# Performance work log

Measured on AMD Instinct MI355X. Metric: run time of the kernel, lower is better.

Reference implementation:

```python
import jax, jax.numpy as jnp
import numpy as np

B, D, U = 8192, 512, 512


def setup_inputs() -> dict:
    key = jax.random.key(0)
    ks = jax.random.split(key, 5)
    return {
        "inputs": jax.random.normal(ks[0], (B, D), dtype=jnp.float32),
        "h_tm1": jax.random.normal(ks[1], (B, U), dtype=jnp.float32),
        "c_tm1": jax.random.normal(ks[2], (B, U), dtype=jnp.float32),
        "kernel": jax.random.normal(ks[3], (D, 4 * U), dtype=jnp.float32) * (1.0 / np.sqrt(D)),
        "recurrent_kernel": jax.random.normal(ks[4], (U, 4 * U), dtype=jnp.float32) * (1.0 / np.sqrt(U)),
        "bias": jnp.zeros((4 * U,), dtype=jnp.float32),
    }


def reference(inputs, h_tm1, c_tm1, kernel, recurrent_kernel, bias):
    # z: [B, 4U] = x @ W + h @ R + b
    z = inputs @ kernel + h_tm1 @ recurrent_kernel + bias
    z0, z1, z2, z3 = jnp.split(z, 4, axis=1)
    i = jax.nn.sigmoid(z0)
    f = jax.nn.sigmoid(z1)
    g = jnp.tanh(z2)
    o = jax.nn.sigmoid(z3)
    c = f * c_tm1 + i * g
    h = o * jnp.tanh(c)
    return (h, h, c)
```

## Files before the change

### kernel.cpp

```cpp
#include <hip/hip_runtime.h>
#include <hip/hip_bf16.h>
#include <cstdint>
#include <cstddef>

#define BB 8192
#define UU 512
#define KPACK 1024
#define NPACK 2048

using frag16 = __attribute__((ext_vector_type(8))) short;
using f32x4  = __attribute__((ext_vector_type(4))) float;

__device__ inline float fast_sigmoid(float x) { return 1.0f / (1.0f + __expf(-x)); }
__device__ inline float fast_tanh(float x) {
  x = fminf(fmaxf(x, -15.f), 15.f);
  float e = __expf(-2.0f * x);
  return (1.0f - e) / (1.0f + e);
}

__device__ inline unsigned cvt2(float lo, float hi) {
  __hip_bfloat162 b = __float22bfloat162_rn(float2{lo, hi});
  union { __hip_bfloat162 b; unsigned u; } v; v.b = b;
  return v.u;
}

__global__ __launch_bounds__(256) void pack_kernel(const float* __restrict__ x,
                                                   const float* __restrict__ h,
                                                   const float* __restrict__ W,
                                                   const float* __restrict__ R,
                                                   short* __restrict__ Xp,
                                                   short* __restrict__ Bt) {
  if (blockIdx.x < 4096) {
    int idx = blockIdx.x * 256 + threadIdx.x;
    int row = idx >> 7;
    int k8  = (idx & 127) << 3;
    const float* src = (k8 < 512) ? (x + (size_t)row * 512 + k8)
                                  : (h + (size_t)row * 512 + (k8 - 512));
    float4 a = *(const float4*)(src);
    float4 b = *(const float4*)(src + 4);
    uint4 o;
    o.x = cvt2(a.x, a.y);
    o.y = cvt2(a.z, a.w);
    o.z = cvt2(b.x, b.y);
    o.w = cvt2(b.z, b.w);
    *(uint4*)(Xp + ((size_t)idx << 3)) = o;
  } else {
    __shared__ float tile[64][65];
    int b2 = blockIdx.x - 4096;
    int nb = (b2 & 31) * 64;
    int kb = (b2 >> 5) * 64;
    int t  = threadIdx.x;
#pragma unroll
    for (int rep = 0; rep < 16; ++rep) {
      int kr = rep * 4 + (t >> 6);
      int c  = t & 63;
      int kg = kb + kr;
      const float* s = (kg < 512) ? (W + (size_t)kg * 2048) : (R + (size_t)(kg - 512) * 2048);
      tile[c][kr] = s[nb + c];
    }
    __syncthreads();
#pragma unroll
    for (int rep = 0; rep < 4; ++rep) {
      int nn = rep * 16 + (t >> 4);
      int k4 = (t & 15) << 2;
      uint2 o;
      o.x = cvt2(tile[nn][k4 + 0], tile[nn][k4 + 1]);
      o.y = cvt2(tile[nn][k4 + 2], tile[nn][k4 + 3]);
      *(uint2*)(Bt + (size_t)(nb + nn) * 1024 + kb + k4) = o;
    }
  }
}

__global__ __launch_bounds__(256, 4) void lstm_mfma_kernel(
    const short* __restrict__ A,
    const short* __restrict__ Bt,
    const float* __restrict__ bias,
    const float* __restrict__ cprev,
    float* __restrict__ out)
{
  __shared__ short lds_a[128 * 64];
  __shared__ short lds_b[128 * 64];

  const int tid  = threadIdx.x;
  const int lane = tid & 63;
  const int wave = tid >> 6;
  const int wm = wave & 1, wn = wave >> 1;
  const int bm = blockIdx.x;
  const int bn = blockIdx.y;

  const int r8  = lane >> 3;
  const int kg  = lane & 7;
  const int kgx = kg ^ r8;

  const short* ga[4];
  const short* gb[4];
  int ls_off[4];
#pragma unroll
  for (int t = 0; t < 4; ++t) {
    int rowl = wave * 32 + t * 8 + r8;
    ga[t] = A + (size_t)(bm * 128 + rowl) * 1024 + kgx * 8;
    int u    = bn * 32 + ((rowl >> 6) << 4) + (rowl & 15);
    int gate = (rowl >> 4) & 3;
    gb[t] = Bt + (size_t)(gate * 512 + u) * 1024 + kgx * 8;
    ls_off[t] = (wave * 32 + t * 8) * 64;
  }

  const int q   = lane >> 4;
  const int c16 = lane & 15;
  const int mx  = c16 & 7;

  f32x4 acc[4][4];
#pragma unroll
  for (int i = 0; i < 4; ++i)
#pragma unroll
    for (int j = 0; j < 4; ++j)
      acc[i][j] = f32x4{0.f, 0.f, 0.f, 0.f};

  for (int kt = 0; kt < 16; ++kt) {
    const int k0 = kt * 64;
#pragma unroll
    for (int t = 0; t < 4; ++t)
      __builtin_amdgcn_global_load_lds(
          (const __attribute__((address_space(1))) void*)(ga[t] + k0),
          (__attribute__((address_space(3))) void*)(lds_a + ls_off[t]), 16, 0, 0);
#pragma unroll
    for (int t = 0; t < 4; ++t)
      __builtin_amdgcn_global_load_lds(
          (const __attribute__((address_space(1))) void*)(gb[t] + k0),
          (__attribute__((address_space(3))) void*)(lds_b + ls_off[t]), 16, 0, 0);
    __syncthreads();
#pragma unroll
    for (int s = 0; s < 2; ++s) {
      const int kch = (((s << 2) + q) ^ mx) << 3;
      frag16 af[4], bf[4];
#pragma unroll
      for (int i = 0; i < 4; ++i)
        af[i] = *(const frag16*)(lds_a + (wm * 64 + i * 16 + c16) * 64 + kch);
#pragma unroll
      for (int j = 0; j < 4; ++j)
        bf[j] = *(const frag16*)(lds_b + (wn * 64 + j * 16 + c16) * 64 + kch);
#pragma unroll
      for (int i = 0; i < 4; ++i)
#pragma unroll
        for (int j = 0; j < 4; ++j)
          acc[i][j] = __builtin_amdgcn_mfma_f32_16x16x32_bf16(af[i], bf[j], acc[i][j], 0, 0, 0);
    }
    __syncthreads();
  }

  const int u = bn * 32 + wn * 16 + c16;
  const float b0 = bias[u];
  const float b1 = bias[512 + u];
  const float b2 = bias[1024 + u];
  const float b3 = bias[1536 + u];
  float* outh0 = out;
  float* outh1 = out + (size_t)BB * UU;
  float* outc  = out + (size_t)2 * BB * UU;

#pragma unroll
  for (int i = 0; i < 4; ++i) {
    int row0 = bm * 128 + wm * 64 + i * 16 + q * 4;
#pragma unroll
    for (int r = 0; r < 4; ++r) {
      size_t off = (size_t)(row0 + r) * UU + u;
      float z0 = acc[i][0][r] + b0;
      float z1 = acc[i][1][r] + b1;
      float z2 = acc[i][2][r] + b2;
      float z3 = acc[i][3][r] + b3;
      float ig = fast_sigmoid(z0);
      float fg = fast_sigmoid(z1);
      float gg = fast_tanh(z2);
      float og = fast_sigmoid(z3);
      float cp = cprev[off];
      float cc = fg * cp + ig * gg;
      float hh = og * fast_tanh(cc);
      outh0[off] = hh;
      outh1[off] = hh;
      outc[off]  = cc;
    }
  }
}

extern "C" void kernel_launch(void* const* d_in, const int* in_sizes, int n_in,
                              void* d_out, int out_size, void* d_ws, size_t ws_size,
                              hipStream_t stream) {
  const float* x  = (const float*)d_in[0];
  const float* h  = (const float*)d_in[1];
  const float* c  = (const float*)d_in[2];
  const float* W  = (const float*)d_in[3];
  const float* R  = (const float*)d_in[4];
  const float* b  = (const float*)d_in[5];
  float* out = (float*)d_out;

  short* Xp = (short*)d_ws;
  short* Bt = Xp + (size_t)BB * KPACK;

  pack_kernel<<<4608, 256, 0, stream>>>(x, h, W, R, Xp, Bt);
  lstm_mfma_kernel<<<dim3(64, 16), 256, 0, stream>>>(Xp, Bt, b, c, out);
}
```

Before: 148.0 us.

## Triple-buffer LDS with async prefetch and enlarge block tile to 256x128

The GEMM kernel now uses 512-thread blocks covering 256 rows by 128 columns, so each B tile is shared by twice as many A rows. K-tiles are staged through a three-deep LDS ring with global_load_lds prefetch two tiles ahead, governed by vmcnt waits and a single barrier per iteration instead of two syncthreads. MFMA sections are raised in priority with s_setprio. The aim is to hide global load latency and cut B-tile reloads, at the cost of about 144KB of LDS per block, which limits residency, and half as many blocks in the grid.

Result: slower. 154.5 us (+4.4%).

```diff
diff --git a/kernel.cpp b/kernel.cpp
--- a/kernel.cpp
+++ b/kernel.cpp
@@ -71,81 +71,105 @@
   }
 }
 
-__global__ __launch_bounds__(256, 4) void lstm_mfma_kernel(
+__global__ __launch_bounds__(512, 2) void lstm_mfma_kernel(
     const short* __restrict__ A,
     const short* __restrict__ Bt,
     const float* __restrict__ bias,
     const float* __restrict__ cprev,
     float* __restrict__ out)
 {
-  __shared__ short lds_a[128 * 64];
-  __shared__ short lds_b[128 * 64];
+  __shared__ short lds[3 * 24576];
 
   const int tid  = threadIdx.x;
   const int lane = tid & 63;
   const int wave = tid >> 6;
-  const int wm = wave & 1, wn = wave >> 1;
-  const int bm = blockIdx.x;
-  const int bn = blockIdx.y;
+  const int wm   = wave & 3;
+  const int wn   = wave >> 2;
+  const int bm   = blockIdx.x;
+  const int bn   = blockIdx.y;
 
   const int r8  = lane >> 3;
   const int kg  = lane & 7;
   const int kgx = kg ^ r8;
 
   const short* ga[4];
-  const short* gb[4];
-  int ls_off[4];
+  int la_off[4];
 #pragma unroll
   for (int t = 0; t < 4; ++t) {
     int rowl = wave * 32 + t * 8 + r8;
-    ga[t] = A + (size_t)(bm * 128 + rowl) * 1024 + kgx * 8;
+    ga[t] = A + (size_t)(bm * 256 + rowl) * 1024 + kgx * 8;
+    la_off[t] = (wave * 32 + t * 8) * 64;
+  }
+  const short* gb[2];
+  int lb_off[2];
+#pragma unroll
+  for (int t = 0; t < 2; ++t) {
+    int rowl = wave * 16 + t * 8 + r8;
     int u    = bn * 32 + ((rowl >> 6) << 4) + (rowl & 15);
     int gate = (rowl >> 4) & 3;
     gb[t] = Bt + (size_t)(gate * 512 + u) * 1024 + kgx * 8;
-    ls_off[t] = (wave * 32 + t * 8) * 64;
+    lb_off[t] = (wave * 16 + t * 8) * 64;
   }
 
   const int q   = lane >> 4;
   const int c16 = lane & 15;
   const int mx  = c16 & 7;
 
-  f32x4 acc[4][4];
-#pragma unroll
-  for (int i = 0; i < 4; ++i)
-#pragma unroll
-    for (int j = 0; j < 4; ++j)
-      acc[i][j] = f32x4{0.f, 0.f, 0.f, 0.f};
-
-  for (int kt = 0; kt < 16; ++kt) {
-    const int k0 = kt * 64;
+  auto STAGE = [&](int T, int bi) {
+    const int k0 = T * 64;
+    short* base = &lds[bi * 24576];
 #pragma unroll
     for (int t = 0; t < 4; ++t)
       __builtin_amdgcn_global_load_lds(
           (const __attribute__((address_space(1))) void*)(ga[t] + k0),
-          (__attribute__((address_space(3))) void*)(lds_a + ls_off[t]), 16, 0, 0);
-#pragma unroll
-    for (int t = 0; t < 4; ++t)
+          (__attribute__((address_space(3))) void*)(base + la_off[t]), 16, 0, 0);
+#pragma unroll
+    for (int t = 0; t < 2; ++t)
       __builtin_amdgcn_global_load_lds(
           (const __attribute__((address_space(1))) void*)(gb[t] + k0),
-          (__attribute__((address_space(3))) void*)(lds_b + ls_off[t]), 16, 0, 0);
-    __syncthreads();
-#pragma unroll
-    for (int s = 0; s < 2; ++s) {
-      const int kch = (((s << 2) + q) ^ mx) << 3;
-      frag16 af[4], bf[4];
+          (__attribute__((address_space(3))) void*)(base + 16384 + lb_off[t]), 16, 0, 0);
+  };
+
+  f32x4 acc[4][4];
+#pragma unroll
+  for (int i = 0; i < 4; ++i)
+#pragma unroll
+    for (int j = 0; j < 4; ++j)
+      acc[i][j] = f32x4{0.f, 0.f, 0.f, 0.f};
+
+  STAGE(0, 0);
+  STAGE(1, 1);
+
+  int rb = 0;
+  for (int T = 0; T < 16; ++T) {
+    if (T < 15) asm volatile("s_waitcnt vmcnt(6)" ::: "memory");
+    else        asm volatile("s_waitcnt vmcnt(0)" ::: "memory");
+    __builtin_amdgcn_s_barrier();
+    if (T + 2 < 16) {
+      int wb = rb + 2; if (wb >= 3) wb -= 3;
+      STAGE(T + 2, wb);
+    }
+    const short* la = &lds[rb * 24576];
+    const short* lb = la + 16384;
+    __builtin_amdgcn_s_setprio(1);
+#pragma unroll
+    for (int ks = 0; ks < 2; ++ks) {
+      const int ch8 = ((((ks << 2) + q) ^ mx) << 3);
+      frag16 af[4], bfv[4];
 #pragma unroll
       for (int i = 0; i < 4; ++i)
-        af[i] = *(const frag16*)(lds_a + (wm * 64 + i * 16 + c16) * 64 + kch);
+        af[i] = *(const frag16*)(la + (wm * 64 + i * 16 + c16) * 64 + ch8);
 #pragma unroll
       for (int j = 0; j < 4; ++j)
-        bf[j] = *(const frag16*)(lds_b + (wn * 64 + j * 16 + c16) * 64 + kch);
+        bfv[j] = *(const frag16*)(lb + (wn * 64 + j * 16 + c16) * 64 + ch8);
 #pragma unroll
       for (int i = 0; i < 4; ++i)
 #pragma unroll
         for (int j = 0; j < 4; ++j)
-          acc[i][j] = __builtin_amdgcn_mfma_f32_16x16x32_bf16(af[i], bf[j], acc[i][j], 0, 0, 0);
-    }
-    __syncthreads();
+          acc[i][j] = __builtin_amdgcn_mfma_f32_16x16x32_bf16(af[i], bfv[j], acc[i][j], 0, 0, 0);
+    }
+    __builtin_amdgcn_s_setprio(0);
+    rb = (rb == 2) ? 0 : rb + 1;
   }
 
   const int u = bn * 32 + wn * 16 + c16;
@@ -159,7 +183,7 @@
 
 #pragma unroll
   for (int i = 0; i < 4; ++i) {
-    int row0 = bm * 128 + wm * 64 + i * 16 + q * 4;
+    int row0 = bm * 256 + wm * 64 + i * 16 + q * 4;
 #pragma unroll
     for (int r = 0; r < 4; ++r) {
       size_t off = (size_t)(row0 + r) * UU + u;
@@ -196,5 +220,5 @@
   short* Bt = Xp + (size_t)BB * KPACK;
 
   pack_kernel<<<4608, 256, 0, stream>>>(x, h, W, R, Xp, Bt);
-  lstm_mfma_kernel<<<dim3(64, 16), 256, 0, stream>>>(Xp, Bt, b, c, out);
-}
+  lstm_mfma_kernel<<<dim3(32, 16), 512, 0, stream>>>(Xp, Bt, b, c, out);
+}
```

## Double-buffer LDS with K-tile 32 to overlap global loads with MFMA

Applied to the files above, without the earlier changes.

The GEMM main loop now uses two LDS buffers with K-tile 32 instead of one buffer with K-tile 64. The next tile's direct-to-LDS loads are issued before the current tile's MFMAs, waiting only with a partial vmcnt so loads overlap compute. A new XOR-swizzled layout packs two rows per 64-element line to keep LDS reads conflict-free. The cost is twice as many loop iterations and barriers. Synchronisation now depends on hand-placed s_barrier and vmcnt waits, which leaves correctness hinging on the exact count of outstanding loads.

After: 154.4 us. +4.3%, slower.

```diff
diff --git a/kernel.cpp b/kernel.cpp
--- a/kernel.cpp
+++ b/kernel.cpp
@@ -78,8 +78,7 @@
     const float* __restrict__ cprev,
     float* __restrict__ out)
 {
-  __shared__ short lds_a[128 * 64];
-  __shared__ short lds_b[128 * 64];
+  __shared__ short lds[2 * 8192];
 
   const int tid  = threadIdx.x;
   const int lane = tid & 63;
@@ -88,26 +87,47 @@
   const int bm = blockIdx.x;
   const int bn = blockIdx.y;
 
-  const int r8  = lane >> 3;
-  const int kg  = lane & 7;
-  const int kgx = kg ^ r8;
-
-  const short* ga[4];
-  const short* gb[4];
-  int ls_off[4];
-#pragma unroll
-  for (int t = 0; t < 4; ++t) {
-    int rowl = wave * 32 + t * 8 + r8;
-    ga[t] = A + (size_t)(bm * 128 + rowl) * 1024 + kgx * 8;
-    int u    = bn * 32 + ((rowl >> 6) << 4) + (rowl & 15);
-    int gate = (rowl >> 4) & 3;
-    gb[t] = Bt + (size_t)(gate * 512 + u) * 1024 + kgx * 8;
-    ls_off[t] = (wave * 32 + t * 8) * 64;
-  }
+  const int l8   = lane >> 3;
+  const int sl   = lane & 7;
+  const int slin = sl ^ l8;
+  const int rpar = slin >> 2;
+  const int cch  = slin & 3;
+
+  const short* ga0[2];
+  const short* gb0[2];
+  int la_off[2], lb_off[2];
+#pragma unroll
+  for (int i = 0; i < 2; ++i) {
+    int g    = wave * 2 + i;
+    int rloc = g * 16 + 2 * l8 + rpar;
+    ga0[i]    = A + (size_t)(bm * 128 + rloc) * 1024 + cch * 8;
+    la_off[i] = g * 512;
+    int u    = bn * 32 + ((rloc >> 6) << 4) + (rloc & 15);
+    int gate = (rloc >> 4) & 3;
+    gb0[i]    = Bt + (size_t)(gate * 512 + u) * 1024 + cch * 8;
+    lb_off[i] = 4096 + g * 512;
+  }
+
+  auto STAGE = [&](int kt, int bi) {
+    const int k0 = kt * 32;
+    short* base = &lds[bi * 8192];
+#pragma unroll
+    for (int i = 0; i < 2; ++i)
+      __builtin_amdgcn_global_load_lds(
+          (const __attribute__((address_space(1))) void*)(ga0[i] + k0),
+          (__attribute__((address_space(3))) void*)(base + la_off[i]), 16, 0, 0);
+#pragma unroll
+    for (int i = 0; i < 2; ++i)
+      __builtin_amdgcn_global_load_lds(
+          (const __attribute__((address_space(1))) void*)(gb0[i] + k0),
+          (__attribute__((address_space(3))) void*)(base + lb_off[i]), 16, 0, 0);
+  };
 
   const int q   = lane >> 4;
   const int c16 = lane & 15;
-  const int mx  = c16 & 7;
+  const int s_rd  = (((c16 & 1) << 2) | q) ^ (c16 >> 1);
+  const int aoff  = wm * 2048 + (c16 >> 1) * 64 + s_rd * 8;
+  const int boff  = 4096 + wn * 2048 + (c16 >> 1) * 64 + s_rd * 8;
 
   f32x4 acc[4][4];
 #pragma unroll
@@ -116,37 +136,33 @@
     for (int j = 0; j < 4; ++j)
       acc[i][j] = f32x4{0.f, 0.f, 0.f, 0.f};
 
-  for (int kt = 0; kt < 16; ++kt) {
-    const int k0 = kt * 64;
-#pragma unroll
-    for (int t = 0; t < 4; ++t)
-      __builtin_amdgcn_global_load_lds(
-          (const __attribute__((address_space(1))) void*)(ga[t] + k0),
-          (__attribute__((address_space(3))) void*)(lds_a + ls_off[t]), 16, 0, 0);
-#pragma unroll
-    for (int t = 0; t < 4; ++t)
-      __builtin_amdgcn_global_load_lds(
-          (const __attribute__((address_space(1))) void*)(gb[t] + k0),
-          (__attribute__((address_space(3))) void*)(lds_b + ls_off[t]), 16, 0, 0);
-    __syncthreads();
-#pragma unroll
-    for (int s = 0; s < 2; ++s) {
-      const int kch = (((s << 2) + q) ^ mx) << 3;
-      frag16 af[4], bf[4];
-#pragma unroll
-      for (int i = 0; i < 4; ++i)
-        af[i] = *(const frag16*)(lds_a + (wm * 64 + i * 16 + c16) * 64 + kch);
+  auto COMPUTE = [&](int kt) {
+    const short* base = &lds[(kt & 1) * 8192];
+    frag16 af[4], bfv[4];
+#pragma unroll
+    for (int i = 0; i < 4; ++i)
+      af[i] = *(const frag16*)(base + aoff + i * 512);
+#pragma unroll
+    for (int j = 0; j < 4; ++j)
+      bfv[j] = *(const frag16*)(base + boff + j * 512);
+#pragma unroll
+    for (int i = 0; i < 4; ++i)
 #pragma unroll
       for (int j = 0; j < 4; ++j)
-        bf[j] = *(const frag16*)(lds_b + (wn * 64 + j * 16 + c16) * 64 + kch);
-#pragma unroll
-      for (int i = 0; i < 4; ++i)
-#pragma unroll
-        for (int j = 0; j < 4; ++j)
-          acc[i][j] = __builtin_amdgcn_mfma_f32_16x16x32_bf16(af[i], bf[j], acc[i][j], 0, 0, 0);
-    }
-    __syncthreads();
-  }
+        acc[i][j] = __builtin_amdgcn_mfma_f32_16x16x32_bf16(af[i], bfv[j], acc[i][j], 0, 0, 0);
+  };
+
+  STAGE(0, 0);
+  for (int kt = 0; kt < 31; ++kt) {
+    __builtin_amdgcn_s_barrier();
+    STAGE(kt + 1, (kt + 1) & 1);
+    asm volatile("s_waitcnt vmcnt(4)" ::: "memory");
+    __builtin_amdgcn_s_barrier();
+    COMPUTE(kt);
+  }
+  asm volatile("s_waitcnt vmcnt(0)" ::: "memory");
+  __builtin_amdgcn_s_barrier();
+  COMPUTE(31);
 
   const int u = bn * 32 + wn * 16 + c16;
   const float b0 = bias[u];
```
